# Optimization experiments

Measured on AMD Instinct MI355X. Metric: run time of the kernel, lower is better.

Reference implementation:

```python
import jax, jax.numpy as jnp
import numpy as np

GRID = 64
ECC = 10.0
ATT_CTR = (3.0, 0.0)
NORM_SIGMA = 0.5


def _grids():
    coords = jnp.linspace(-ECC, ECC, GRID, dtype=jnp.float32)
    X, Y = jnp.meshgrid(coords, coords)          # (64,64)
    RF_X = X.reshape(-1)                         # (4096,) one RF center per grid point
    RF_Y = Y.reshape(-1)
    return X, Y, RF_X, RF_Y


def _fields(X, Y, RF_X, RF_Y, sigma):
    # Batched Gaussian fields: (64,64,4096), each normalized to unit sum.
    d2 = (X[:, :, None] - RF_X) ** 2 + (Y[:, :, None] - RF_Y) ** 2
    g = jnp.exp(-d2 / (2.0 * sigma ** 2))
    return g / jnp.sum(g, axis=(0, 1), keepdims=True)


def setup_inputs() -> dict:
    key = jax.random.key(0)
    ks = jax.random.split(key, 2)
    stim = jax.random.uniform(ks[0], (GRID, GRID, 256), dtype=jnp.float32)
    return {
        "stim": stim,
        "prf_sigma_scale_factor": jnp.float32(0.2),
        "attention_field_sigma": jnp.float32(2.0),
        "attention_field_gain": jnp.float32(4.0),
        "suppressive_surround_sigma_factor": jnp.float32(3.0),
        "summation_field_sigma_factor": jnp.float32(2.0),
    }


def reference(stim, prf_sigma_scale_factor, attention_field_sigma,
              attention_field_gain, suppressive_surround_sigma_factor,
              summation_field_sigma_factor):
    X, Y, RF_X, RF_Y = _grids()
    if stim.ndim != 3:
        stim = stim[:, :, None]

    # Attention field: unnormalized Gaussian, flattened, gain*g + 1.
    att = jnp.exp(-((X - ATT_CTR[0]) ** 2 + (Y - ATT_CTR[1]) ** 2)
                  / (2.0 * attention_field_sigma ** 2)).reshape(-1)  # (4096,)
    attfield = attention_field_gain * att + 1.0

    rf_sigma = 0.07 + prf_sigma_scale_factor * jnp.sqrt(RF_X ** 2 + RF_Y ** 2)  # (4096,)

    receptive_field = _fields(X, Y, RF_X, RF_Y, rf_sigma)                                  # (64,64,4096)
    suppressive_surround = _fields(X, Y, RF_X, RF_Y, rf_sigma * suppressive_surround_sigma_factor).reshape(GRID * GRID, -1)
    summation_field = _fields(X, Y, RF_X, RF_Y, rf_sigma * summation_field_sigma_factor).reshape(GRID * GRID, -1)

    stimulus_drive = jnp.einsum('ijk,ija->ka', receptive_field, stim)   # (4096, a)
    numerator = stimulus_drive * attfield[:, None]                      # (4096, a)
    surroundresponse = suppressive_surround.T @ numerator               # (4096, a)
    predicted_neural = numerator / (surroundresponse + NORM_SIGMA)
    predicted_voxel = summation_field.T @ predicted_neural
    # voxel_lookup_indices is identity (voxeldata=None), so lookups are no-ops.
    return (numerator, surroundresponse, predicted_neural, predicted_voxel)
```

## Files before the change

kernel.cpp:

```cpp
#include <hip/hip_runtime.h>
#include <hip/hip_bf16.h>
#include <math.h>

#define NP 4096
#define NA 256

typedef unsigned short ushort_t;
typedef __attribute__((ext_vector_type(8))) short short8;
typedef __attribute__((ext_vector_type(4))) float f32x4;
typedef __attribute__((ext_vector_type(8))) unsigned short ushort8v;

__device__ __forceinline__ ushort_t f2bf(float x) {
    __hip_bfloat16 h = __float2bfloat16(x);
    return *reinterpret_cast<ushort_t*>(&h);
}
__device__ __forceinline__ float bf2f(ushort_t u) {
    unsigned x = ((unsigned)u) << 16;
    return __builtin_bit_cast(float, x);
}

__device__ __forceinline__ short8 pack_row(const float* rp) {
    f32x4 v0 = *(const f32x4*)(rp);
    f32x4 v1 = *(const f32x4*)(rp + 4);
    short8 r;
    r[0] = (short)f2bf(v0[0]); r[1] = (short)f2bf(v0[1]);
    r[2] = (short)f2bf(v0[2]); r[3] = (short)f2bf(v0[3]);
    r[4] = (short)f2bf(v1[0]); r[5] = (short)f2bf(v1[1]);
    r[6] = (short)f2bf(v1[2]); r[7] = (short)f2bf(v1[3]);
    return r;
}

__global__ __launch_bounds__(512)
void transpose_stim(const float* __restrict__ stim, ushort_t* __restrict__ stimT)
{
    __shared__ float lt[64 * 68];
    const int t = threadIdx.x;
    const int v = blockIdx.x;
    const int g0 = (v & 63) * 64, a0 = (v >> 6) * 64;
    const int gr = t >> 3, ar = (t & 7) * 8;
    *(f32x4*)&lt[gr * 68 + ar]     = *(const f32x4*)&stim[(size_t)(g0 + gr) * NA + a0 + ar];
    *(f32x4*)&lt[gr * 68 + ar + 4] = *(const f32x4*)&stim[(size_t)(g0 + gr) * NA + a0 + ar + 4];
    __syncthreads();
    const int a = t >> 3, c8 = (t & 7) * 8;
    ushort8v u;
    #pragma unroll
    for (int i = 0; i < 8; ++i) u[i] = f2bf(lt[(c8 + i) * 68 + a]);
    *(ushort8v*)&stimT[(size_t)(a0 + a) * NP + g0 + c8] = u;
}

template <int MODE>
__global__ __launch_bounds__(512)
void field_gemm(const ushort_t* __restrict__ bT,
                const float* __restrict__ pscale,
                const float* __restrict__ pasig,
                const float* __restrict__ pagain,
                const float* __restrict__ pssf,
                const float* __restrict__ psff,
                const float* __restrict__ num,
                float* __restrict__ C,
                float* __restrict__ C2,
                ushort_t* __restrict__ CT,
                const ushort_t* __restrict__ numTsrc)
{
    __shared__ __align__(16) unsigned char smem[147712];
    ushort_t* lB   = (ushort_t*)smem;
    float*    lgx  = (float*)(smem + 98304);
    float*    lgy2 = (float*)(smem + 131072);
    float*    latt = (float*)(smem + 147456);

    const int t    = threadIdx.x;
    const int w    = t >> 6;
    const int l    = t & 63;
    const int asub = w >> 1;
    const int kh   = w & 1;
    const int r16  = l & 15;
    const int q    = l >> 4;
    const int srow  = l >> 3;
    const int sslot = (l & 7) ^ (srow & 7);

    const int v   = blockIdx.x;
    const int lid = (v & 7) * 32 + (v >> 3);
    const int p0  = (lid & 63) * 64;
    const int a0  = (lid >> 6) * 64;

    const float sc_scale = pscale[0];
    const float fac = (MODE == 0) ? 1.0f : (MODE == 1 ? pssf[0] : psff[0]);

#define STAGE(buf, tt)                                                         \
    _Pragma("unroll")                                                          \
    for (int h = 0; h < 2; ++h) {                                              \
        const ushort_t* src = bT + (size_t)(a0 + w * 8 + srow) * NP            \
                              + (2 * (tt) + h) * 64 + sslot * 8;               \
        ushort_t* dst = lB + ((buf) * 2 + h) * 4096 + (w * 8) * 64;            \
        __builtin_amdgcn_global_load_lds(                                      \
            (const __attribute__((address_space(1))) unsigned int*)src,        \
            (__attribute__((address_space(3))) unsigned int*)dst, 16, 0, 0);   \
    }

    STAGE(0, 0); STAGE(1, 1); STAGE(2, 2); STAGE(3, 3);

    const float step = 20.0f / 63.0f;
    const float coord = -10.0f + step * (float)l;
    #pragma unroll
    for (int i = 0; i < 8; ++i) {
        const int pl = w * 8 + i, p = p0 + pl;
        float cx = -10.0f + step * (float)(p & 63);
        float cy = -10.0f + step * (float)(p >> 6);
        float sg = (0.07f + sc_scale * sqrtf(cx * cx + cy * cy)) * fac;
        float inv = 1.0f / (2.0f * sg * sg);
        float dx = coord - cx, dy = coord - cy;
        float ex = expf(-dx * dx * inv);
        float ey = expf(-dy * dy * inv);
        float sx = ex, sy = ey;
        #pragma unroll
        for (int o = 32; o > 0; o >>= 1) {
            sx += __shfl_xor(sx, o);
            sy += __shfl_xor(sy, o);
        }
        lgx[pl * 64 + l] = ex / sx;
        lgy2[l * 64 + (((pl & 15) * 4) ^ ((l & 7) << 3)) + (pl >> 4)] = ey / sy;
        if (MODE == 0 && l == 0) {
            float asig = pasig[0];
            float d2 = (cx - 3.0f) * (cx - 3.0f) + cy * cy;
            latt[pl] = pagain[0] * expf(-d2 / (2.0f * asig * asig)) + 1.0f;
        }
    }
    __syncthreads();

    short8 gxf[4][2];
    #pragma unroll
    for (int pt = 0; pt < 4; ++pt) {
        const float* rowp = lgx + (size_t)(pt * 16 + r16) * 64;
        gxf[pt][0] = pack_row(rowp + q * 8);
        gxf[pt][1] = pack_row(rowp + 32 + q * 8);
    }
    asm volatile("s_waitcnt lgkmcnt(0)" ::: "memory");
    __builtin_amdgcn_sched_barrier(0);

    const int n   = asub * 16 + r16;
    const int bo0 = n * 64 + ((q ^ (n & 7)) * 8);
    const int bo1 = n * 64 + (((4 + q) ^ (n & 7)) * 8);

    f32x4 acc[4];
    #pragma unroll
    for (int pt = 0; pt < 4; ++pt) acc[pt] = (f32x4){0.f, 0.f, 0.f, 0.f};

    for (int ph = 0; ph < 16; ++ph) {
        if (ph <= 13) {
            STAGE((2 * ph + 4) & 7, 2 * ph + 4);
            STAGE((2 * ph + 5) & 7, 2 * ph + 5);
            asm volatile("s_waitcnt vmcnt(8)" ::: "memory");
        } else if (ph == 14) {
            asm volatile("s_waitcnt vmcnt(4)" ::: "memory");
        } else {
            asm volatile("s_waitcnt vmcnt(0)" ::: "memory");
        }
        __builtin_amdgcn_s_barrier();

        #pragma unroll
        for (int u = 0; u < 2; ++u) {
            const int tt = 2 * ph + u;
            const ushort_t* bb = lB + ((tt & 7) * 2 + kh) * 4096;
            short8 A0 = *(const short8*)(bb + bo0);
            short8 A1 = *(const short8*)(bb + bo1);
            const int gi = 2 * tt + kh;
            f32x4 s4 = *(const f32x4*)(lgy2 + gi * 64 +
                                       ((r16 * 4) ^ ((gi & 7) << 3)));
            __builtin_amdgcn_s_setprio(1);
            #pragma unroll
            for (int pt = 0; pt < 4; ++pt) {
                f32x4 tmp = (f32x4){0.f, 0.f, 0.f, 0.f};
                tmp = __builtin_amdgcn_mfma_f32_16x16x32_bf16(A0, gxf[pt][0], tmp, 0, 0, 0);
                tmp = __builtin_amdgcn_mfma_f32_16x16x32_bf16(A1, gxf[pt][1], tmp, 0, 0, 0);
                float sc = s4[pt];
                acc[pt] += tmp * sc;
            }
            __builtin_amdgcn_s_setprio(0);
        }
    }
#undef STAGE

    __syncthreads();
    float* lred_ap = (float*)smem;
    float* lred_pa = (float*)(smem + 34816);

    const int a_base = asub * 16 + q * 4;
    #pragma unroll
    for (int pt = 0; pt < 4; ++pt) {
        const int p_idx = pt * 16 + r16;
        *(f32x4*)&lred_pa[(kh * 64 + p_idx) * 68 + a_base] = acc[pt];
        #pragma unroll
        for (int r = 0; r < 4; ++r)
            lred_ap[(kh * 64 + a_base + r) * 68 + p_idx] = acc[pt][r];
    }
    __syncthreads();

    if (MODE != 2) {
        const int aL = t >> 3, p8 = (t & 7) * 8;
        f32x4 s0 = *(f32x4*)&lred_ap[aL * 68 + p8] +
                   *(f32x4*)&lred_ap[(64 + aL) * 68 + p8];
        f32x4 s1 = *(f32x4*)&lred_ap[aL * 68 + p8 + 4] +
                   *(f32x4*)&lred_ap[(64 + aL) * 68 + p8 + 4];
        ushort8v cv;
        if (MODE == 0) {
            f32x4 t0 = *(f32x4*)&latt[p8];
            f32x4 t1 = *(f32x4*)&latt[p8 + 4];
            s0 *= t0; s1 *= t1;
            #pragma unroll
            for (int r = 0; r < 4; ++r) {
                cv[r] = f2bf(s0[r]);
                cv[4 + r] = f2bf(s1[r]);
            }
        } else {
            ushort8v nt = *(const ushort8v*)&numTsrc[(size_t)(a0 + aL) * NP + p0 + p8];
            #pragma unroll
            for (int r = 0; r < 4; ++r) {
                cv[r] = f2bf(bf2f(nt[r]) / (s0[r] + 0.5f));
                cv[4 + r] = f2bf(bf2f(nt[4 + r]) / (s1[r] + 0.5f));
            }
        }
        *(ushort8v*)&CT[(size_t)(a0 + aL) * NP + p0 + p8] = cv;
    }

    {
        const int pL = t >> 3, a8 = (t & 7) * 8;
        f32x4 s0 = *(f32x4*)&lred_pa[pL * 68 + a8] +
                   *(f32x4*)&lred_pa[(64 + pL) * 68 + a8];
        f32x4 s1 = *(f32x4*)&lred_pa[pL * 68 + a8 + 4] +
                   *(f32x4*)&lred_pa[(64 + pL) * 68 + a8 + 4];
        float* cbase = C + (size_t)(p0 + pL) * NA + a0 + a8;
        if (MODE == 0) {
            float att = latt[pL];
            s0 *= att; s1 *= att;
            *(f32x4*)cbase = s0;
            *(f32x4*)(cbase + 4) = s1;
        } else if (MODE == 1) {
            *(f32x4*)cbase = s0;
            *(f32x4*)(cbase + 4) = s1;
            const float* nb = num + (size_t)(p0 + pL) * NA + a0 + a8;
            f32x4 n0 = *(const f32x4*)nb;
            f32x4 n1 = *(const f32x4*)(nb + 4);
            f32x4 o0 = n0 / (s0 + 0.5f);
            f32x4 o1 = n1 / (s1 + 0.5f);
            float* c2 = C2 + (size_t)(p0 + pL) * NA + a0 + a8;
            *(f32x4*)c2 = o0;
            *(f32x4*)(c2 + 4) = o1;
        } else {
            *(f32x4*)cbase = s0;
            *(f32x4*)(cbase + 4) = s1;
        }
    }
}

extern "C" void kernel_launch(void* const* d_in, const int* in_sizes, int n_in,
                              void* d_out, int out_size, void* d_ws, size_t ws_size,
                              hipStream_t stream)
{
    const float* stim   = (const float*)d_in[0];
    const float* pscale = (const float*)d_in[1];
    const float* pasig  = (const float*)d_in[2];
    const float* pagain = (const float*)d_in[3];
    const float* pssf   = (const float*)d_in[4];
    const float* psff   = (const float*)d_in[5];

    float* out  = (float*)d_out;
    float* num  = out;
    float* surr = out + (size_t)NP * NA;
    float* pn   = out + 2 * (size_t)NP * NA;
    float* pv   = out + 3 * (size_t)NP * NA;

    ushort_t* stimT = (ushort_t*)d_ws;
    ushort_t* numT  = stimT + (size_t)NA * NP;
    ushort_t* pnT   = numT + (size_t)NA * NP;

    transpose_stim<<<256, 512, 0, stream>>>(stim, stimT);

    field_gemm<0><<<256, 512, 0, stream>>>(stimT, pscale, pasig, pagain, pssf,
                                           psff, nullptr, num, nullptr, numT,
                                           nullptr);
    field_gemm<1><<<256, 512, 0, stream>>>(numT, pscale, pasig, pagain, pssf,
                                           psff, num, surr, pn, pnT, numT);
    field_gemm<2><<<256, 512, 0, stream>>>(pnT, pscale, pasig, pagain, pssf,
                                           psff, nullptr, pv, nullptr, nullptr,
                                           nullptr);
}
```

Baseline: 69.29 us.

## Precompute separable Gaussian field factors in setup kernel and stream them into GEMMs

Moves the per-block computation of the separable Gaussian x/y factors (and the attention field) out of each field_gemm launch into a single setup kernel that also does the stim transpose. The GEMM kernels then load the precomputed bf16 gx fragments straight from global memory and pull the gy tables and attention values into LDS with async global_load_lds. This removes the exp, shuffle-reduction and conversion work from the GEMM prologue, in exchange for extra workspace traffic and a larger setup launch. The factors are still computed on every call, so no work is skipped.

New measurement: 65.52 us. -5.4%, faster.

```diff
diff --git a/kernel.cpp b/kernel.cpp
--- a/kernel.cpp
+++ b/kernel.cpp
@@ -19,43 +19,79 @@
     return __builtin_bit_cast(float, x);
 }
 
-__device__ __forceinline__ short8 pack_row(const float* rp) {
-    f32x4 v0 = *(const f32x4*)(rp);
-    f32x4 v1 = *(const f32x4*)(rp + 4);
-    short8 r;
-    r[0] = (short)f2bf(v0[0]); r[1] = (short)f2bf(v0[1]);
-    r[2] = (short)f2bf(v0[2]); r[3] = (short)f2bf(v0[3]);
-    r[4] = (short)f2bf(v1[0]); r[5] = (short)f2bf(v1[1]);
-    r[6] = (short)f2bf(v1[2]); r[7] = (short)f2bf(v1[3]);
-    return r;
-}
-
 __global__ __launch_bounds__(512)
-void transpose_stim(const float* __restrict__ stim, ushort_t* __restrict__ stimT)
+void setup_all(const float* __restrict__ stim,
+               const float* __restrict__ pscale,
+               const float* __restrict__ pasig,
+               const float* __restrict__ pagain,
+               const float* __restrict__ pssf,
+               const float* __restrict__ psff,
+               ushort_t* __restrict__ stimT,
+               ushort_t* __restrict__ gxbI,
+               float* __restrict__ gy2I,
+               float* __restrict__ attI)
 {
     __shared__ float lt[64 * 68];
     const int t = threadIdx.x;
-    const int v = blockIdx.x;
-    const int g0 = (v & 63) * 64, a0 = (v >> 6) * 64;
-    const int gr = t >> 3, ar = (t & 7) * 8;
-    *(f32x4*)&lt[gr * 68 + ar]     = *(const f32x4*)&stim[(size_t)(g0 + gr) * NA + a0 + ar];
-    *(f32x4*)&lt[gr * 68 + ar + 4] = *(const f32x4*)&stim[(size_t)(g0 + gr) * NA + a0 + ar + 4];
-    __syncthreads();
-    const int a = t >> 3, c8 = (t & 7) * 8;
-    ushort8v u;
-    #pragma unroll
-    for (int i = 0; i < 8; ++i) u[i] = f2bf(lt[(c8 + i) * 68 + a]);
-    *(ushort8v*)&stimT[(size_t)(a0 + a) * NP + g0 + c8] = u;
+    const int bx = blockIdx.x;
+    const float step = 20.0f / 63.0f;
+
+    if (bx < 256) {
+        const int g0 = (bx & 63) * 64, a0 = (bx >> 6) * 64;
+        const int gr = t >> 3, ar = (t & 7) * 8;
+        *(f32x4*)&lt[gr * 68 + ar]     = *(const f32x4*)&stim[(size_t)(g0 + gr) * NA + a0 + ar];
+        *(f32x4*)&lt[gr * 68 + ar + 4] = *(const f32x4*)&stim[(size_t)(g0 + gr) * NA + a0 + ar + 4];
+        __syncthreads();
+        const int a = t >> 3, c8 = (t & 7) * 8;
+        ushort8v u;
+        #pragma unroll
+        for (int i = 0; i < 8; ++i) u[i] = f2bf(lt[(c8 + i) * 68 + a]);
+        *(ushort8v*)&stimT[(size_t)(a0 + a) * NP + g0 + c8] = u;
+    } else {
+        const int b    = bx - 256;
+        const int f    = b >> 6;
+        const int pblk = b & 63;
+        const int w    = t >> 6;
+        const int l    = t & 63;
+        const float sc_scale = pscale[0];
+        const float fac = (f == 0) ? 1.0f : (f == 1 ? pssf[0] : psff[0]);
+        const float coord = -10.0f + step * (float)l;
+        ushort_t* gxb = gxbI + ((size_t)f * 64 + pblk) * 4096;
+        float*    gy2 = gy2I + ((size_t)f * 64 + pblk) * 4096;
+
+        #pragma unroll
+        for (int i = 0; i < 8; ++i) {
+            const int pl = w * 8 + i, p = pblk * 64 + pl;
+            float cx = -10.0f + step * (float)(p & 63);
+            float cy = -10.0f + step * (float)(p >> 6);
+            float sg = (0.07f + sc_scale * sqrtf(cx * cx + cy * cy)) * fac;
+            float inv = 1.0f / (2.0f * sg * sg);
+            float dx = coord - cx, dy = coord - cy;
+            float ex = expf(-dx * dx * inv);
+            float ey = expf(-dy * dy * inv);
+            float sx = ex, sy = ey;
+            #pragma unroll
+            for (int o = 32; o > 0; o >>= 1) {
+                sx += __shfl_xor(sx, o);
+                sy += __shfl_xor(sy, o);
+            }
+            gxb[pl * 64 + l] = f2bf(ex / sx);
+            gy2[l * 64 + (((pl & 15) * 4) ^ ((l & 7) << 3)) + (pl >> 4)] = ey / sy;
+            if (f == 0 && l == 0) {
+                float asig = pasig[0];
+                float d2 = (cx - 3.0f) * (cx - 3.0f) + cy * cy;
+                attI[p] = pagain[0] * expf(-d2 / (2.0f * asig * asig)) + 1.0f;
+            }
+        }
+    }
 }
 
 template <int MODE>
 __global__ __launch_bounds__(512)
 void field_gemm(const ushort_t* __restrict__ bT,
-                const float* __restrict__ pscale,
-                const float* __restrict__ pasig,
-                const float* __restrict__ pagain,
-                const float* __restrict__ pssf,
-                const float* __restrict__ psff,
+                const ushort_t* __restrict__ gxbF,
+                const float* __restrict__ gy2F,
+                const float* __restrict__ attI,
                 const float* __restrict__ num,
                 float* __restrict__ C,
                 float* __restrict__ C2,
@@ -64,7 +100,6 @@
 {
     __shared__ __align__(16) unsigned char smem[147712];
     ushort_t* lB   = (ushort_t*)smem;
-    float*    lgx  = (float*)(smem + 98304);
     float*    lgy2 = (float*)(smem + 131072);
     float*    latt = (float*)(smem + 147456);
 
@@ -78,13 +113,11 @@
     const int srow  = l >> 3;
     const int sslot = (l & 7) ^ (srow & 7);
 
-    const int v   = blockIdx.x;
-    const int lid = (v & 7) * 32 + (v >> 3);
-    const int p0  = (lid & 63) * 64;
-    const int a0  = (lid >> 6) * 64;
-
-    const float sc_scale = pscale[0];
-    const float fac = (MODE == 0) ? 1.0f : (MODE == 1 ? pssf[0] : psff[0]);
+    const int v    = blockIdx.x;
+    const int lid  = (v & 7) * 32 + (v >> 3);
+    const int pblk = lid & 63;
+    const int p0   = pblk * 64;
+    const int a0   = (lid >> 6) * 64;
 
 #define STAGE(buf, tt)                                                         \
     _Pragma("unroll")                                                          \
@@ -99,43 +132,34 @@
 
     STAGE(0, 0); STAGE(1, 1); STAGE(2, 2); STAGE(3, 3);
 
-    const float step = 20.0f / 63.0f;
-    const float coord = -10.0f + step * (float)l;
-    #pragma unroll
-    for (int i = 0; i < 8; ++i) {
-        const int pl = w * 8 + i, p = p0 + pl;
-        float cx = -10.0f + step * (float)(p & 63);
-        float cy = -10.0f + step * (float)(p >> 6);
-        float sg = (0.07f + sc_scale * sqrtf(cx * cx + cy * cy)) * fac;
-        float inv = 1.0f / (2.0f * sg * sg);
-        float dx = coord - cx, dy = coord - cy;
-        float ex = expf(-dx * dx * inv);
-        float ey = expf(-dy * dy * inv);
-        float sx = ex, sy = ey;
-        #pragma unroll
-        for (int o = 32; o > 0; o >>= 1) {
-            sx += __shfl_xor(sx, o);
-            sy += __shfl_xor(sy, o);
-        }
-        lgx[pl * 64 + l] = ex / sx;
-        lgy2[l * 64 + (((pl & 15) * 4) ^ ((l & 7) << 3)) + (pl >> 4)] = ey / sy;
-        if (MODE == 0 && l == 0) {
-            float asig = pasig[0];
-            float d2 = (cx - 3.0f) * (cx - 3.0f) + cy * cy;
-            latt[pl] = pagain[0] * expf(-d2 / (2.0f * asig * asig)) + 1.0f;
-        }
-    }
-    __syncthreads();
-
+    {
+        const float* gsrc = gy2F + (size_t)pblk * 4096;
+        #pragma unroll
+        for (int r = 0; r < 2; ++r) {
+            const float* src = gsrc + (w * 2 + r) * 256 + l * 4;
+            float* dst = lgy2 + (w * 2 + r) * 256;
+            __builtin_amdgcn_global_load_lds(
+                (const __attribute__((address_space(1))) unsigned int*)src,
+                (__attribute__((address_space(3))) unsigned int*)dst, 16, 0, 0);
+        }
+    }
+    if (MODE == 0 && w == 0) {
+        const float* src = attI + p0 + l;
+        __builtin_amdgcn_global_load_lds(
+            (const __attribute__((address_space(1))) unsigned int*)src,
+            (__attribute__((address_space(3))) unsigned int*)latt, 4, 0, 0);
+    }
+
+    const ushort_t* gxb = gxbF + (size_t)pblk * 4096;
     short8 gxf[4][2];
     #pragma unroll
     for (int pt = 0; pt < 4; ++pt) {
-        const float* rowp = lgx + (size_t)(pt * 16 + r16) * 64;
-        gxf[pt][0] = pack_row(rowp + q * 8);
-        gxf[pt][1] = pack_row(rowp + 32 + q * 8);
-    }
-    asm volatile("s_waitcnt lgkmcnt(0)" ::: "memory");
-    __builtin_amdgcn_sched_barrier(0);
+        const int row = pt * 16 + r16;
+        gxf[pt][0] = *(const short8*)&gxb[row * 64 + q * 8];
+        gxf[pt][1] = *(const short8*)&gxb[row * 64 + 32 + q * 8];
+    }
+
+    __syncthreads();
 
     const int n   = asub * 16 + r16;
     const int bo0 = n * 64 + ((q ^ (n & 7)) * 8);
@@ -272,15 +296,24 @@
     ushort_t* stimT = (ushort_t*)d_ws;
     ushort_t* numT  = stimT + (size_t)NA * NP;
     ushort_t* pnT   = numT + (size_t)NA * NP;
-
-    transpose_stim<<<256, 512, 0, stream>>>(stim, stimT);
-
-    field_gemm<0><<<256, 512, 0, stream>>>(stimT, pscale, pasig, pagain, pssf,
-                                           psff, nullptr, num, nullptr, numT,
-                                           nullptr);
-    field_gemm<1><<<256, 512, 0, stream>>>(numT, pscale, pasig, pagain, pssf,
-                                           psff, num, surr, pn, pnT, numT);
-    field_gemm<2><<<256, 512, 0, stream>>>(pnT, pscale, pasig, pagain, pssf,
-                                           psff, nullptr, pv, nullptr, nullptr,
-                                           nullptr);
-}
+    ushort_t* gxbI  = pnT + (size_t)NA * NP;
+    float*    gy2I  = (float*)(gxbI + (size_t)3 * 64 * 4096);
+    float*    attI  = gy2I + (size_t)3 * 64 * 4096;
+
+    setup_all<<<448, 512, 0, stream>>>(stim, pscale, pasig, pagain, pssf, psff,
+                                       stimT, gxbI, gy2I, attI);
+
+    const ushort_t* gx0 = gxbI;
+    const ushort_t* gx1 = gxbI + (size_t)64 * 4096;
+    const ushort_t* gx2 = gxbI + (size_t)128 * 4096;
+    const float*    gy0 = gy2I;
+    const float*    gy1 = gy2I + (size_t)64 * 4096;
+    const float*    gy2 = gy2I + (size_t)128 * 4096;
+
+    field_gemm<0><<<256, 512, 0, stream>>>(stimT, gx0, gy0, attI, nullptr,
+                                           num, nullptr, numT, nullptr);
+    field_gemm<1><<<256, 512, 0, stream>>>(numT, gx1, gy1, attI, num,
+                                           surr, pn, pnT, numT);
+    field_gemm<2><<<256, 512, 0, stream>>>(pnT, gx2, gy2, attI, nullptr,
+                                           pv, nullptr, nullptr, nullptr);
+}
```
